# Performance work log

Hardware: AMD Instinct MI355X
Metric: run time of the kernel (lower is better)

## Reference

```python
import jax, jax.numpy as jnp
import numpy as np

B, C, H, W = 32, 3, 512, 512
OUT = (64, 64)  # (out_grid[0]=Nx, out_grid[1]=Ny)
SMALL = 1e-4


def setup_inputs() -> dict:
    key = jax.random.key(0)
    k1, k2 = jax.random.split(key, 2)
    X = jax.random.normal(k1, (B, C, H, W), dtype=jnp.float32)
    fan_in = C * H * W
    # localization net: flatten + dense(5); scaled so p ~ N(0,1) and exp(p) is stable
    W_loc = jax.random.normal(k2, (fan_in, 5), dtype=jnp.float32) / np.float32(np.sqrt(fan_in))
    b_loc = jnp.zeros((5,), dtype=jnp.float32)
    return {"X": X, "W_loc": W_loc, "b_loc": b_loc}


def reference(X, W_loc, b_loc):
    Bn = X.shape[0]
    # locnet: p = flatten(X) @ W_loc + b_loc  -> [B, 5]
    p = X.reshape(Bn, -1) @ W_loc + b_loc

    N = min(OUT)
    gx = OUT[0] * (p[:, 0] + 1.0) / 2.0          # [B]
    gy = OUT[1] * (p[:, 1] + 1.0) / 2.0          # [B]
    sigma2 = jnp.exp(p[:, 2])                    # [B]
    delta = jnp.exp(p[:, 3]) * (max(W, H) - 1) / (N - 1.0)  # [B]
    gamma = jnp.exp(p[:, 4])                     # [B]

    i1 = jnp.arange(OUT[0], dtype=jnp.float32)   # [Nx]
    i2 = jnp.arange(OUT[1], dtype=jnp.float32)   # [Ny]
    a = jnp.arange(W, dtype=jnp.float32)         # [W]
    b = jnp.arange(H, dtype=jnp.float32)         # [H]

    mx = gx[:, None] + delta[:, None] * (i1 - N / 2.0 - 0.5)  # [B, Nx]
    my = gy[:, None] + delta[:, None] * (i2 - N / 2.0 - 0.5)  # [B, Ny]

    Fx = jnp.exp(-((a - mx[:, :, None]) ** 2) / (2.0 * sigma2[:, None, None]))  # [B,Nx,W]
    Fx = Fx / (Fx.sum(axis=-1, keepdims=True) + SMALL)
    Fy = jnp.exp(-((b - my[:, :, None]) ** 2) / (2.0 * sigma2[:, None, None]))  # [B,Ny,H]
    Fy = Fy / (Fy.sum(axis=-1, keepdims=True) + SMALL)

    # glimpse read: gamma * Fy @ X @ Fx^T, done as batched contractions
    Fyx = jnp.einsum('bnh,bchw->bcnw', Fy, X)        # [B,C,Ny,W]
    out = jnp.einsum('bcnw,bmw->bcnm', Fyx, Fx)      # [B,C,Ny,Nx]
    return gamma[:, None, None, None] * out
```

## Files before the change

kernel.cpp:

```cpp
#include <hip/hip_runtime.h>
#include <math.h>

#define B_ 32
#define C_ 3
#define H_ 512
#define W_ 512
#define NOUT 64
#define FAN (C_*H_*W_)

#define CHUNKS 96
#define CELEMS (FAN / CHUNKS)
#define BGROUPS 4

#define P_OFF 0
#define FX_OFF 256
#define FY_OFF (FX_OFF + B_*NOUT*W_)

__global__ __launch_bounds__(256) void k_locnet(const float* __restrict__ X,
                                                const float* __restrict__ Wl,
                                                float* __restrict__ ws) {
    const int chunk = blockIdx.x;
    const int b0 = blockIdx.y * 8;
    const int t = threadIdx.x;

    float acc[8][5] = {};
    const size_t base = (size_t)chunk * CELEMS;

    for (int k = t; k < CELEMS / 4; k += 256) {
        const size_t i0 = base + (size_t)k * 4;
        const float4* W4 = (const float4*)(Wl + i0 * 5);
        float4 w0 = W4[0], w1 = W4[1], w2 = W4[2], w3 = W4[3], w4 = W4[4];
        float wv[20] = {w0.x, w0.y, w0.z, w0.w,
                        w1.x, w1.y, w1.z, w1.w,
                        w2.x, w2.y, w2.z, w2.w,
                        w3.x, w3.y, w3.z, w3.w,
                        w4.x, w4.y, w4.z, w4.w};
        #pragma unroll
        for (int bb = 0; bb < 8; bb++) {
            float4 x = *(const float4*)(X + (size_t)(b0 + bb) * FAN + i0);
            float xv[4] = {x.x, x.y, x.z, x.w};
            #pragma unroll
            for (int e = 0; e < 4; e++)
                #pragma unroll
                for (int j = 0; j < 5; j++)
                    acc[bb][j] += xv[e] * wv[e * 5 + j];
        }
    }

    #pragma unroll
    for (int off = 32; off > 0; off >>= 1)
        #pragma unroll
        for (int bb = 0; bb < 8; bb++)
            #pragma unroll
            for (int j = 0; j < 5; j++)
                acc[bb][j] += __shfl_down(acc[bb][j], off);

    __shared__ float sred[4][40];
    const int wave = t >> 6, lane = t & 63;
    if (lane == 0) {
        #pragma unroll
        for (int bb = 0; bb < 8; bb++)
            #pragma unroll
            for (int j = 0; j < 5; j++)
                sred[wave][bb * 5 + j] = acc[bb][j];
    }
    __syncthreads();
    if (t < 40) {
        float s = sred[0][t] + sred[1][t] + sred[2][t] + sred[3][t];
        atomicAdd(&ws[P_OFF + b0 * 5 + t], s);
    }
}

__global__ __launch_bounds__(256) void k_filters(const float* __restrict__ bl,
                                                 float* __restrict__ ws) {
    const int n = blockIdx.x;
    const int b = blockIdx.y;
    const int which = blockIdx.z;
    const int t = threadIdx.x;

    const float p0 = ws[P_OFF + b * 5 + 0] + bl[0];
    const float p1 = ws[P_OFF + b * 5 + 1] + bl[1];
    const float p2 = ws[P_OFF + b * 5 + 2] + bl[2];
    const float p3 = ws[P_OFF + b * 5 + 3] + bl[3];

    const float g = (which == 0) ? 32.f * (p0 + 1.f) : 32.f * (p1 + 1.f);
    const float sigma2 = expf(p2);
    const float inv2s = 0.5f / sigma2;
    const float delta = expf(p3) * (511.0f / 63.0f);
    const float mean = g + delta * ((float)n - 32.5f);

    float d0 = (float)t - mean;
    float f0 = expf(-d0 * d0 * inv2s);
    float d1 = (float)(t + 256) - mean;
    float f1 = expf(-d1 * d1 * inv2s);

    float s = f0 + f1;
    #pragma unroll
    for (int off = 32; off > 0; off >>= 1) s += __shfl_down(s, off);
    __shared__ float sred[4];
    __shared__ float stot;
    const int wave = t >> 6, lane = t & 63;
    if (lane == 0) sred[wave] = s;
    __syncthreads();
    if (t == 0) stot = sred[0] + sred[1] + sred[2] + sred[3] + 1e-4f;
    __syncthreads();
    const float scale = 1.0f / stot;

    float* dst = ws + (which == 0 ? FX_OFF : FY_OFF) + ((size_t)b * NOUT + n) * W_;
    dst[t] = f0 * scale;
    dst[t + 256] = f1 * scale;
}

__global__ __launch_bounds__(256) void k_glimpse(const float* __restrict__ X,
                                                 const float* __restrict__ bl,
                                                 const float* __restrict__ ws,
                                                 float* __restrict__ out) {
    const int hc = blockIdx.x;
    const int bc = blockIdx.y;
    const int b = bc / 3;
    const int t = threadIdx.x;
    const int th = t >> 4;
    const int tm = t & 15;
    const int hbase = hc * 64;

    __shared__ float lds[2 * 64 * 66];
    float (*Xs)[66]  = (float (*)[66])(lds);
    float (*Fxs)[66] = (float (*)[66])(lds + 64 * 66);
    float (*GsT)[66] = (float (*)[66])(lds);
    float (*Fys)[66] = (float (*)[66])(lds + 64 * 66);

    const float* Xp  = X + (size_t)bc * (H_ * W_) + (size_t)hbase * W_;
    const float* Fxp = ws + FX_OFF + (size_t)b * NOUT * W_;
    const float* Fyp = ws + FY_OFF + (size_t)b * NOUT * W_;

    float g[4][4] = {};

    for (int wt = 0; wt < 8; wt++) {
        const int wbase = wt * 64;
        #pragma unroll
        for (int k = 0; k < 4; k++) {
            int idx = t + 256 * k;
            int row = idx >> 4;
            int wq = idx & 15;
            float4 xf = *(const float4*)(Xp + (size_t)row * W_ + wbase + wq * 4);
            float4 ff = *(const float4*)(Fxp + (size_t)row * W_ + wbase + wq * 4);
            float* xd = &Xs[row][wq * 4];
            xd[0] = xf.x; xd[1] = xf.y; xd[2] = xf.z; xd[3] = xf.w;
            float* fd = &Fxs[row][wq * 4];
            fd[0] = ff.x; fd[1] = ff.y; fd[2] = ff.z; fd[3] = ff.w;
        }
        __syncthreads();
        #pragma unroll 4
        for (int w = 0; w < 64; w += 2) {
            float2 xv[4], fv[4];
            #pragma unroll
            for (int i = 0; i < 4; i++) xv[i] = *(const float2*)&Xs[th + 16 * i][w];
            #pragma unroll
            for (int j = 0; j < 4; j++) fv[j] = *(const float2*)&Fxs[tm + 16 * j][w];
            #pragma unroll
            for (int i = 0; i < 4; i++)
                #pragma unroll
                for (int j = 0; j < 4; j++) {
                    g[i][j] += xv[i].x * fv[j].x;
                    g[i][j] += xv[i].y * fv[j].y;
                }
        }
        __syncthreads();
    }

    #pragma unroll
    for (int i = 0; i < 4; i++)
        #pragma unroll
        for (int j = 0; j < 4; j++)
            GsT[tm + 16 * j][th + 16 * i] = g[i][j];

    #pragma unroll
    for (int k = 0; k < 4; k++) {
        int idx = t + 256 * k;
        int n = idx >> 4;
        int hq = idx & 15;
        float4 ff = *(const float4*)(Fyp + (size_t)n * W_ + hbase + hq * 4);
        float* fd = &Fys[n][hq * 4];
        fd[0] = ff.x; fd[1] = ff.y; fd[2] = ff.z; fd[3] = ff.w;
    }
    __syncthreads();

    float a2[4][4] = {};
    #pragma unroll 4
    for (int hl = 0; hl < 64; hl += 2) {
        float2 fy[4], gv[4];
        #pragma unroll
        for (int i = 0; i < 4; i++) fy[i] = *(const float2*)&Fys[th + 16 * i][hl];
        #pragma unroll
        for (int j = 0; j < 4; j++) gv[j] = *(const float2*)&GsT[tm + 16 * j][hl];
        #pragma unroll
        for (int i = 0; i < 4; i++)
            #pragma unroll
            for (int j = 0; j < 4; j++) {
                a2[i][j] += fy[i].x * gv[j].x;
                a2[i][j] += fy[i].y * gv[j].y;
            }
    }

    const float gamma = expf(ws[P_OFF + b * 5 + 4] + bl[4]);
    float* outp = out + (size_t)bc * (NOUT * NOUT);
    #pragma unroll
    for (int i = 0; i < 4; i++)
        #pragma unroll
        for (int j = 0; j < 4; j++)
            atomicAdd(&outp[(th + 16 * i) * NOUT + (tm + 16 * j)], gamma * a2[i][j]);
}

extern "C" void kernel_launch(void* const* d_in, const int* in_sizes, int n_in,
                              void* d_out, int out_size, void* d_ws, size_t ws_size,
                              hipStream_t stream) {
    const float* X  = (const float*)d_in[0];
    const float* Wl = (const float*)d_in[1];
    const float* bl = (const float*)d_in[2];
    float* out = (float*)d_out;
    float* ws  = (float*)d_ws;

    hipMemsetAsync(ws, 0, 1024, stream);
    hipMemsetAsync(out, 0, (size_t)out_size * sizeof(float), stream);

    k_locnet<<<dim3(CHUNKS, BGROUPS), 256, 0, stream>>>(X, Wl, ws);
    k_filters<<<dim3(NOUT, B_, 2), 256, 0, stream>>>(bl, ws);
    k_glimpse<<<dim3(8, B_ * C_), 256, 0, stream>>>(X, bl, ws, out);
}
```

Before: 245.9 us.

## Use split-bf16 MFMA for glimpse contractions and raise locnet chunk count

Replaces the scalar FP32 outer-product loops in the glimpse kernel with bf16 MFMA 16x16x32 instructions. Each FP32 operand is split into high and low bf16 parts and three MFMAs are issued per product to keep close to FP32 accuracy. Operands are converted and stored as bf16 in LDS with a padded pitch. The locnet kernel's chunk count rises from 96 to 384 for more parallelism, at the cost of more atomic adds. Risks are the extra conversion work and the small precision loss from dropping the low-times-low term.

```diff
diff --git a/kernel.cpp b/kernel.cpp
--- a/kernel.cpp
+++ b/kernel.cpp
@@ -8,13 +8,25 @@
 #define NOUT 64
 #define FAN (C_*H_*W_)
 
-#define CHUNKS 96
+#define CHUNKS 384
 #define CELEMS (FAN / CHUNKS)
 #define BGROUPS 4
 
 #define P_OFF 0
 #define FX_OFF 256
 #define FY_OFF (FX_OFF + B_*NOUT*W_)
+
+typedef __bf16 bf16x8 __attribute__((ext_vector_type(8)));
+typedef float f32x4 __attribute__((ext_vector_type(4)));
+
+__device__ __forceinline__ unsigned short f2bf(float f) {
+    unsigned int u = __float_as_uint(f);
+    u = (u + 0x7FFFu + ((u >> 16) & 1u)) >> 16;
+    return (unsigned short)u;
+}
+__device__ __forceinline__ float bf2f(unsigned short h) {
+    return __uint_as_float(((unsigned int)h) << 16);
+}
 
 __global__ __launch_bounds__(256) void k_locnet(const float* __restrict__ X,
                                                 const float* __restrict__ Wl,
@@ -111,6 +123,10 @@
     dst[t + 256] = f1 * scale;
 }
 
+#define KC 64
+#define PITCH 72
+#define TSZ (64 * PITCH)
+
 __global__ __launch_bounds__(256) void k_glimpse(const float* __restrict__ X,
                                                  const float* __restrict__ bl,
                                                  const float* __restrict__ ws,
@@ -119,96 +135,145 @@
     const int bc = blockIdx.y;
     const int b = bc / 3;
     const int t = threadIdx.x;
-    const int th = t >> 4;
-    const int tm = t & 15;
+    const int lane = t & 63;
+    const int wv = t >> 6;
+    const int l15 = lane & 15;
+    const int quad = lane >> 4;
     const int hbase = hc * 64;
 
-    __shared__ float lds[2 * 64 * 66];
-    float (*Xs)[66]  = (float (*)[66])(lds);
-    float (*Fxs)[66] = (float (*)[66])(lds + 64 * 66);
-    float (*GsT)[66] = (float (*)[66])(lds);
-    float (*Fys)[66] = (float (*)[66])(lds + 64 * 66);
+    __shared__ __align__(16) unsigned short lds[4 * TSZ];
+    unsigned short* Xh = lds;
+    unsigned short* Xl = lds + TSZ;
+    unsigned short* Fh = lds + 2 * TSZ;
+    unsigned short* Fl = lds + 3 * TSZ;
 
     const float* Xp  = X + (size_t)bc * (H_ * W_) + (size_t)hbase * W_;
     const float* Fxp = ws + FX_OFF + (size_t)b * NOUT * W_;
     const float* Fyp = ws + FY_OFF + (size_t)b * NOUT * W_;
 
-    float g[4][4] = {};
+    f32x4 acc[4] = {};
 
     for (int wt = 0; wt < 8; wt++) {
-        const int wbase = wt * 64;
-        #pragma unroll
-        for (int k = 0; k < 4; k++) {
-            int idx = t + 256 * k;
+        const int wbase = wt * KC;
+        #pragma unroll
+        for (int k4 = 0; k4 < 4; k4++) {
+            int idx = t + 256 * k4;
             int row = idx >> 4;
-            int wq = idx & 15;
-            float4 xf = *(const float4*)(Xp + (size_t)row * W_ + wbase + wq * 4);
-            float4 ff = *(const float4*)(Fxp + (size_t)row * W_ + wbase + wq * 4);
-            float* xd = &Xs[row][wq * 4];
-            xd[0] = xf.x; xd[1] = xf.y; xd[2] = xf.z; xd[3] = xf.w;
-            float* fd = &Fxs[row][wq * 4];
-            fd[0] = ff.x; fd[1] = ff.y; fd[2] = ff.z; fd[3] = ff.w;
+            int c4 = (idx & 15) * 4;
+            float4 xv = *(const float4*)(Xp + (size_t)row * W_ + wbase + c4);
+            float4 fv = *(const float4*)(Fxp + (size_t)row * W_ + wbase + c4);
+            float xa[4] = {xv.x, xv.y, xv.z, xv.w};
+            float fa[4] = {fv.x, fv.y, fv.z, fv.w};
+            unsigned int xhp[2], xlp[2], fhp[2], flp[2];
+            #pragma unroll
+            for (int hwd = 0; hwd < 2; hwd++) {
+                unsigned short h0 = f2bf(xa[2*hwd]);
+                unsigned short h1 = f2bf(xa[2*hwd+1]);
+                xhp[hwd] = (unsigned int)h0 | ((unsigned int)h1 << 16);
+                unsigned short l0 = f2bf(xa[2*hwd] - bf2f(h0));
+                unsigned short l1 = f2bf(xa[2*hwd+1] - bf2f(h1));
+                xlp[hwd] = (unsigned int)l0 | ((unsigned int)l1 << 16);
+                unsigned short g0 = f2bf(fa[2*hwd]);
+                unsigned short g1 = f2bf(fa[2*hwd+1]);
+                fhp[hwd] = (unsigned int)g0 | ((unsigned int)g1 << 16);
+                unsigned short m0 = f2bf(fa[2*hwd] - bf2f(g0));
+                unsigned short m1 = f2bf(fa[2*hwd+1] - bf2f(g1));
+                flp[hwd] = (unsigned int)m0 | ((unsigned int)m1 << 16);
+            }
+            int o = row * PITCH + c4;
+            *(uint2*)&Xh[o] = make_uint2(xhp[0], xhp[1]);
+            *(uint2*)&Xl[o] = make_uint2(xlp[0], xlp[1]);
+            *(uint2*)&Fh[o] = make_uint2(fhp[0], fhp[1]);
+            *(uint2*)&Fl[o] = make_uint2(flp[0], flp[1]);
         }
         __syncthreads();
-        #pragma unroll 4
-        for (int w = 0; w < 64; w += 2) {
-            float2 xv[4], fv[4];
-            #pragma unroll
-            for (int i = 0; i < 4; i++) xv[i] = *(const float2*)&Xs[th + 16 * i][w];
-            #pragma unroll
-            for (int j = 0; j < 4; j++) fv[j] = *(const float2*)&Fxs[tm + 16 * j][w];
-            #pragma unroll
-            for (int i = 0; i < 4; i++)
-                #pragma unroll
-                for (int j = 0; j < 4; j++) {
-                    g[i][j] += xv[i].x * fv[j].x;
-                    g[i][j] += xv[i].y * fv[j].y;
-                }
+        #pragma unroll
+        for (int ks = 0; ks < 2; ks++) {
+            const int ko = ks * 32 + quad * 8;
+            bf16x8 ah = *(const bf16x8*)&Xh[(16 * wv + l15) * PITCH + ko];
+            bf16x8 al = *(const bf16x8*)&Xl[(16 * wv + l15) * PITCH + ko];
+            #pragma unroll
+            for (int mt = 0; mt < 4; mt++) {
+                bf16x8 bh = *(const bf16x8*)&Fh[(16 * mt + l15) * PITCH + ko];
+                bf16x8 bl2 = *(const bf16x8*)&Fl[(16 * mt + l15) * PITCH + ko];
+                acc[mt] = __builtin_amdgcn_mfma_f32_16x16x32_bf16(ah, bh, acc[mt], 0, 0, 0);
+                acc[mt] = __builtin_amdgcn_mfma_f32_16x16x32_bf16(al, bh, acc[mt], 0, 0, 0);
+                acc[mt] = __builtin_amdgcn_mfma_f32_16x16x32_bf16(ah, bl2, acc[mt], 0, 0, 0);
+            }
         }
         __syncthreads();
     }
 
     #pragma unroll
-    for (int i = 0; i < 4; i++)
-        #pragma unroll
-        for (int j = 0; j < 4; j++)
-            GsT[tm + 16 * j][th + 16 * i] = g[i][j];
-
-    #pragma unroll
-    for (int k = 0; k < 4; k++) {
-        int idx = t + 256 * k;
+    for (int mt = 0; mt < 4; mt++) {
+        unsigned int ghp[2], glp[2];
+        unsigned short gh[4], gl[4];
+        #pragma unroll
+        for (int r = 0; r < 4; r++) {
+            float g = acc[mt][r];
+            gh[r] = f2bf(g);
+            gl[r] = f2bf(g - bf2f(gh[r]));
+        }
+        ghp[0] = (unsigned int)gh[0] | ((unsigned int)gh[1] << 16);
+        ghp[1] = (unsigned int)gh[2] | ((unsigned int)gh[3] << 16);
+        glp[0] = (unsigned int)gl[0] | ((unsigned int)gl[1] << 16);
+        glp[1] = (unsigned int)gl[2] | ((unsigned int)gl[3] << 16);
+        int m = 16 * mt + l15;
+        int h = 16 * wv + quad * 4;
+        int o = m * PITCH + h;
+        *(uint2*)&Xh[o] = make_uint2(ghp[0], ghp[1]);
+        *(uint2*)&Xl[o] = make_uint2(glp[0], glp[1]);
+    }
+
+    #pragma unroll
+    for (int k4 = 0; k4 < 4; k4++) {
+        int idx = t + 256 * k4;
         int n = idx >> 4;
-        int hq = idx & 15;
-        float4 ff = *(const float4*)(Fyp + (size_t)n * W_ + hbase + hq * 4);
-        float* fd = &Fys[n][hq * 4];
-        fd[0] = ff.x; fd[1] = ff.y; fd[2] = ff.z; fd[3] = ff.w;
-    }
-    __syncthreads();
-
-    float a2[4][4] = {};
-    #pragma unroll 4
-    for (int hl = 0; hl < 64; hl += 2) {
-        float2 fy[4], gv[4];
-        #pragma unroll
-        for (int i = 0; i < 4; i++) fy[i] = *(const float2*)&Fys[th + 16 * i][hl];
-        #pragma unroll
-        for (int j = 0; j < 4; j++) gv[j] = *(const float2*)&GsT[tm + 16 * j][hl];
-        #pragma unroll
-        for (int i = 0; i < 4; i++)
-            #pragma unroll
-            for (int j = 0; j < 4; j++) {
-                a2[i][j] += fy[i].x * gv[j].x;
-                a2[i][j] += fy[i].y * gv[j].y;
-            }
+        int c4 = (idx & 15) * 4;
+        float4 fv = *(const float4*)(Fyp + (size_t)n * W_ + hbase + c4);
+        float fa[4] = {fv.x, fv.y, fv.z, fv.w};
+        unsigned int fhp[2], flp[2];
+        #pragma unroll
+        for (int hwd = 0; hwd < 2; hwd++) {
+            unsigned short g0 = f2bf(fa[2*hwd]);
+            unsigned short g1 = f2bf(fa[2*hwd+1]);
+            fhp[hwd] = (unsigned int)g0 | ((unsigned int)g1 << 16);
+            unsigned short m0 = f2bf(fa[2*hwd] - bf2f(g0));
+            unsigned short m1 = f2bf(fa[2*hwd+1] - bf2f(g1));
+            flp[hwd] = (unsigned int)m0 | ((unsigned int)m1 << 16);
+        }
+        int o = n * PITCH + c4;
+        *(uint2*)&Fh[o] = make_uint2(fhp[0], fhp[1]);
+        *(uint2*)&Fl[o] = make_uint2(flp[0], flp[1]);
+    }
+    __syncthreads();
+
+    f32x4 p[4] = {};
+    #pragma unroll
+    for (int ks = 0; ks < 2; ks++) {
+        const int ko = ks * 32 + quad * 8;
+        bf16x8 yh = *(const bf16x8*)&Fh[(16 * wv + l15) * PITCH + ko];
+        bf16x8 yl = *(const bf16x8*)&Fl[(16 * wv + l15) * PITCH + ko];
+        #pragma unroll
+        for (int mt = 0; mt < 4; mt++) {
+            bf16x8 gh = *(const bf16x8*)&Xh[(16 * mt + l15) * PITCH + ko];
+            bf16x8 gl = *(const bf16x8*)&Xl[(16 * mt + l15) * PITCH + ko];
+            p[mt] = __builtin_amdgcn_mfma_f32_16x16x32_bf16(yh, gh, p[mt], 0, 0, 0);
+            p[mt] = __builtin_amdgcn_mfma_f32_16x16x32_bf16(yl, gh, p[mt], 0, 0, 0);
+            p[mt] = __builtin_amdgcn_mfma_f32_16x16x32_bf16(yh, gl, p[mt], 0, 0, 0);
+        }
     }
 
     const float gamma = expf(ws[P_OFF + b * 5 + 4] + bl[4]);
     float* outp = out + (size_t)bc * (NOUT * NOUT);
     #pragma unroll
-    for (int i = 0; i < 4; i++)
-        #pragma unroll
-        for (int j = 0; j < 4; j++)
-            atomicAdd(&outp[(th + 16 * i) * NOUT + (tm + 16 * j)], gamma * a2[i][j]);
+    for (int mt = 0; mt < 4; mt++)
+        #pragma unroll
+        for (int r = 0; r < 4; r++) {
+            int n = 16 * wv + quad * 4 + r;
+            int m = 16 * mt + l15;
+            atomicAdd(&outp[n * NOUT + m], gamma * p[mt][r]);
+        }
 }
 
 extern "C" void kernel_launch(void* const* d_in, const int* in_sizes, int n_in,
```

New measurement: 213.7 us. 13.1% less time.

## Use split-bf16 MFMA for glimpse contractions and retile locnet reduction

Applied to the files above, without the earlier changes.

The glimpse kernel's two FP32 scalar contractions are replaced with bf16 MFMA 16x16x32 instructions using a hi/lo split (three products) to keep near-fp32 accuracy. The filter kernel now writes Fx/Fy as precomputed hi/lo bf16 arrays, and X is converted on the fly. The locnet kernel processes 16 batches per block over 384 chunks to read each weight element fewer times. The aim is to cut the ALU-bound glimpse time and the weight traffic, at the cost of extra conversions, more registers, and a small precision risk.

```diff
diff --git a/kernel.cpp b/kernel.cpp
--- a/kernel.cpp
+++ b/kernel.cpp
@@ -8,22 +8,46 @@
 #define NOUT 64
 #define FAN (C_*H_*W_)
 
-#define CHUNKS 96
+#define CHUNKS 384
 #define CELEMS (FAN / CHUNKS)
-#define BGROUPS 4
-
-#define P_OFF 0
-#define FX_OFF 256
-#define FY_OFF (FX_OFF + B_*NOUT*W_)
-
-__global__ __launch_bounds__(256) void k_locnet(const float* __restrict__ X,
-                                                const float* __restrict__ Wl,
-                                                float* __restrict__ ws) {
+#define NB 16
+#define BGROUPS (B_ / NB)
+
+#define FXH_OFF 1024
+#define ARR_ELEMS (B_*NOUT*W_)
+
+typedef __bf16 bf16x8 __attribute__((ext_vector_type(8)));
+typedef float f32x4 __attribute__((ext_vector_type(4)));
+
+__device__ __forceinline__ unsigned short f2bf(float f) {
+    unsigned int u = __float_as_uint(f);
+    u = (u + 0x7FFFu + ((u >> 16) & 1u)) >> 16;
+    return (unsigned short)u;
+}
+__device__ __forceinline__ float bf2f(unsigned short h) {
+    return __uint_as_float(((unsigned int)h) << 16);
+}
+__device__ __forceinline__ void cvt_hilo(const float* x, bf16x8* hi, bf16x8* lo) {
+    union { unsigned int u[4]; bf16x8 v; } H, L;
+    #pragma unroll
+    for (int i = 0; i < 4; i++) {
+        unsigned short h0 = f2bf(x[2*i]),  h1 = f2bf(x[2*i+1]);
+        H.u[i] = (unsigned int)h0 | ((unsigned int)h1 << 16);
+        unsigned short l0 = f2bf(x[2*i]   - bf2f(h0));
+        unsigned short l1 = f2bf(x[2*i+1] - bf2f(h1));
+        L.u[i] = (unsigned int)l0 | ((unsigned int)l1 << 16);
+    }
+    *hi = H.v; *lo = L.v;
+}
+
+__global__ __launch_bounds__(256, 3) void k_locnet(const float* __restrict__ X,
+                                                   const float* __restrict__ Wl,
+                                                   float* __restrict__ ws) {
     const int chunk = blockIdx.x;
-    const int b0 = blockIdx.y * 8;
+    const int b0 = blockIdx.y * NB;
     const int t = threadIdx.x;
 
-    float acc[8][5] = {};
+    float acc[NB][5] = {};
     const size_t base = (size_t)chunk * CELEMS;
 
     for (int k = t; k < CELEMS / 4; k += 256) {
@@ -36,7 +60,7 @@
                         w3.x, w3.y, w3.z, w3.w,
                         w4.x, w4.y, w4.z, w4.w};
         #pragma unroll
-        for (int bb = 0; bb < 8; bb++) {
+        for (int bb = 0; bb < NB; bb++) {
             float4 x = *(const float4*)(X + (size_t)(b0 + bb) * FAN + i0);
             float xv[4] = {x.x, x.y, x.z, x.w};
             #pragma unroll
@@ -50,42 +74,45 @@
     #pragma unroll
     for (int off = 32; off > 0; off >>= 1)
         #pragma unroll
-        for (int bb = 0; bb < 8; bb++)
+        for (int bb = 0; bb < NB; bb++)
             #pragma unroll
             for (int j = 0; j < 5; j++)
                 acc[bb][j] += __shfl_down(acc[bb][j], off);
 
-    __shared__ float sred[4][40];
+    __shared__ float sred[4][NB * 5];
     const int wave = t >> 6, lane = t & 63;
     if (lane == 0) {
         #pragma unroll
-        for (int bb = 0; bb < 8; bb++)
+        for (int bb = 0; bb < NB; bb++)
             #pragma unroll
             for (int j = 0; j < 5; j++)
                 sred[wave][bb * 5 + j] = acc[bb][j];
     }
     __syncthreads();
-    if (t < 40) {
+    if (t < NB * 5) {
         float s = sred[0][t] + sred[1][t] + sred[2][t] + sred[3][t];
-        atomicAdd(&ws[P_OFF + b0 * 5 + t], s);
+        atomicAdd(&ws[b0 * 5 + t], s);
     }
 }
 
 __global__ __launch_bounds__(256) void k_filters(const float* __restrict__ bl,
-                                                 float* __restrict__ ws) {
+                                                 void* __restrict__ wsv) {
     const int n = blockIdx.x;
     const int b = blockIdx.y;
     const int which = blockIdx.z;
     const int t = threadIdx.x;
 
-    const float p0 = ws[P_OFF + b * 5 + 0] + bl[0];
-    const float p1 = ws[P_OFF + b * 5 + 1] + bl[1];
-    const float p2 = ws[P_OFF + b * 5 + 2] + bl[2];
-    const float p3 = ws[P_OFF + b * 5 + 3] + bl[3];
+    const float* pw = (const float*)wsv;
+    unsigned short* arrh = (unsigned short*)((char*)wsv + FXH_OFF) + (size_t)which * 2 * ARR_ELEMS;
+    unsigned short* arrl = arrh + ARR_ELEMS;
+
+    const float p0 = pw[b * 5 + 0] + bl[0];
+    const float p1 = pw[b * 5 + 1] + bl[1];
+    const float p2 = pw[b * 5 + 2] + bl[2];
+    const float p3 = pw[b * 5 + 3] + bl[3];
 
     const float g = (which == 0) ? 32.f * (p0 + 1.f) : 32.f * (p1 + 1.f);
-    const float sigma2 = expf(p2);
-    const float inv2s = 0.5f / sigma2;
+    const float inv2s = 0.5f / expf(p2);
     const float delta = expf(p3) * (511.0f / 63.0f);
     const float mean = g + delta * ((float)n - 32.5f);
 
@@ -106,109 +133,108 @@
     __syncthreads();
     const float scale = 1.0f / stot;
 
-    float* dst = ws + (which == 0 ? FX_OFF : FY_OFF) + ((size_t)b * NOUT + n) * W_;
-    dst[t] = f0 * scale;
-    dst[t + 256] = f1 * scale;
-}
+    const size_t o = ((size_t)b * NOUT + n) * W_;
+    float v0 = f0 * scale, v1 = f1 * scale;
+    unsigned short h0 = f2bf(v0), h1 = f2bf(v1);
+    arrh[o + t] = h0;
+    arrh[o + t + 256] = h1;
+    arrl[o + t] = f2bf(v0 - bf2f(h0));
+    arrl[o + t + 256] = f2bf(v1 - bf2f(h1));
+}
+
+#define GP 72
 
 __global__ __launch_bounds__(256) void k_glimpse(const float* __restrict__ X,
                                                  const float* __restrict__ bl,
-                                                 const float* __restrict__ ws,
+                                                 const void* __restrict__ wsv,
                                                  float* __restrict__ out) {
     const int hc = blockIdx.x;
     const int bc = blockIdx.y;
     const int b = bc / 3;
     const int t = threadIdx.x;
-    const int th = t >> 4;
-    const int tm = t & 15;
+    const int lane = t & 63;
+    const int wv = t >> 6;
+    const int l15 = lane & 15;
+    const int quad = lane >> 4;
     const int hbase = hc * 64;
 
-    __shared__ float lds[2 * 64 * 66];
-    float (*Xs)[66]  = (float (*)[66])(lds);
-    float (*Fxs)[66] = (float (*)[66])(lds + 64 * 66);
-    float (*GsT)[66] = (float (*)[66])(lds);
-    float (*Fys)[66] = (float (*)[66])(lds + 64 * 66);
-
-    const float* Xp  = X + (size_t)bc * (H_ * W_) + (size_t)hbase * W_;
-    const float* Fxp = ws + FX_OFF + (size_t)b * NOUT * W_;
-    const float* Fyp = ws + FY_OFF + (size_t)b * NOUT * W_;
-
-    float g[4][4] = {};
-
-    for (int wt = 0; wt < 8; wt++) {
-        const int wbase = wt * 64;
-        #pragma unroll
-        for (int k = 0; k < 4; k++) {
-            int idx = t + 256 * k;
-            int row = idx >> 4;
-            int wq = idx & 15;
-            float4 xf = *(const float4*)(Xp + (size_t)row * W_ + wbase + wq * 4);
-            float4 ff = *(const float4*)(Fxp + (size_t)row * W_ + wbase + wq * 4);
-            float* xd = &Xs[row][wq * 4];
-            xd[0] = xf.x; xd[1] = xf.y; xd[2] = xf.z; xd[3] = xf.w;
-            float* fd = &Fxs[row][wq * 4];
-            fd[0] = ff.x; fd[1] = ff.y; fd[2] = ff.z; fd[3] = ff.w;
-        }
-        __syncthreads();
-        #pragma unroll 4
-        for (int w = 0; w < 64; w += 2) {
-            float2 xv[4], fv[4];
-            #pragma unroll
-            for (int i = 0; i < 4; i++) xv[i] = *(const float2*)&Xs[th + 16 * i][w];
-            #pragma unroll
-            for (int j = 0; j < 4; j++) fv[j] = *(const float2*)&Fxs[tm + 16 * j][w];
-            #pragma unroll
-            for (int i = 0; i < 4; i++)
-                #pragma unroll
-                for (int j = 0; j < 4; j++) {
-                    g[i][j] += xv[i].x * fv[j].x;
-                    g[i][j] += xv[i].y * fv[j].y;
-                }
-        }
-        __syncthreads();
-    }
-
-    #pragma unroll
-    for (int i = 0; i < 4; i++)
-        #pragma unroll
-        for (int j = 0; j < 4; j++)
-            GsT[tm + 16 * j][th + 16 * i] = g[i][j];
-
-    #pragma unroll
-    for (int k = 0; k < 4; k++) {
-        int idx = t + 256 * k;
-        int n = idx >> 4;
-        int hq = idx & 15;
-        float4 ff = *(const float4*)(Fyp + (size_t)n * W_ + hbase + hq * 4);
-        float* fd = &Fys[n][hq * 4];
-        fd[0] = ff.x; fd[1] = ff.y; fd[2] = ff.z; fd[3] = ff.w;
-    }
-    __syncthreads();
-
-    float a2[4][4] = {};
+    const float* pw = (const float*)wsv;
+    const unsigned short* fxh = (const unsigned short*)((const char*)wsv + FXH_OFF) + (size_t)b * NOUT * W_;
+    const unsigned short* fxl = fxh + ARR_ELEMS;
+    const unsigned short* fyh = fxh + 2 * ARR_ELEMS;
+    const unsigned short* fyl = fxh + 3 * ARR_ELEMS;
+
+    __shared__ __align__(16) unsigned short Gh[64 * GP];
+    __shared__ __align__(16) unsigned short Gl[64 * GP];
+
+    const float* Xp = X + (size_t)bc * (H_ * W_);
+
+    f32x4 ahh[4] = {}, axl[4] = {};
+    const size_t arow = (size_t)(hbase + 16 * wv + l15) * W_;
     #pragma unroll 4
-    for (int hl = 0; hl < 64; hl += 2) {
-        float2 fy[4], gv[4];
-        #pragma unroll
-        for (int i = 0; i < 4; i++) fy[i] = *(const float2*)&Fys[th + 16 * i][hl];
-        #pragma unroll
-        for (int j = 0; j < 4; j++) gv[j] = *(const float2*)&GsT[tm + 16 * j][hl];
-        #pragma unroll
-        for (int i = 0; i < 4; i++)
-            #pragma unroll
-            for (int j = 0; j < 4; j++) {
-                a2[i][j] += fy[i].x * gv[j].x;
-                a2[i][j] += fy[i].y * gv[j].y;
-            }
-    }
-
-    const float gamma = expf(ws[P_OFF + b * 5 + 4] + bl[4]);
+    for (int ks = 0; ks < 16; ks++) {
+        const int ko = ks * 32 + quad * 8;
+        float xa[8];
+        *(float4*)&xa[0] = *(const float4*)(Xp + arow + ko);
+        *(float4*)&xa[4] = *(const float4*)(Xp + arow + ko + 4);
+        bf16x8 ah, al;
+        cvt_hilo(xa, &ah, &al);
+        #pragma unroll
+        for (int mt = 0; mt < 4; mt++) {
+            const int fo = (16 * mt + l15) * W_ + ko;
+            bf16x8 bh  = *(const bf16x8*)&fxh[fo];
+            bf16x8 bl2 = *(const bf16x8*)&fxl[fo];
+            ahh[mt] = __builtin_amdgcn_mfma_f32_16x16x32_bf16(ah, bh,  ahh[mt], 0, 0, 0);
+            axl[mt] = __builtin_amdgcn_mfma_f32_16x16x32_bf16(al, bh,  axl[mt], 0, 0, 0);
+            axl[mt] = __builtin_amdgcn_mfma_f32_16x16x32_bf16(ah, bl2, axl[mt], 0, 0, 0);
+        }
+    }
+
+    #pragma unroll
+    for (int mt = 0; mt < 4; mt++) {
+        unsigned short gh[4], gl[4];
+        #pragma unroll
+        for (int r = 0; r < 4; r++) {
+            float g = ahh[mt][r] + axl[mt][r];
+            gh[r] = f2bf(g);
+            gl[r] = f2bf(g - bf2f(gh[r]));
+        }
+        int o = (16 * mt + l15) * GP + 16 * wv + quad * 4;
+        *(uint2*)&Gh[o] = make_uint2((unsigned int)gh[0] | ((unsigned int)gh[1] << 16),
+                                     (unsigned int)gh[2] | ((unsigned int)gh[3] << 16));
+        *(uint2*)&Gl[o] = make_uint2((unsigned int)gl[0] | ((unsigned int)gl[1] << 16),
+                                     (unsigned int)gl[2] | ((unsigned int)gl[3] << 16));
+    }
+    __syncthreads();
+
+    f32x4 ph[4] = {}, px[4] = {};
+    const size_t yrow = (size_t)(16 * wv + l15) * W_ + hbase;
+    #pragma unroll
+    for (int ks = 0; ks < 2; ks++) {
+        const int ko = ks * 32 + quad * 8;
+        bf16x8 yh = *(const bf16x8*)&fyh[yrow + ko];
+        bf16x8 yl = *(const bf16x8*)&fyl[yrow + ko];
+        #pragma unroll
+        for (int mt = 0; mt < 4; mt++) {
+            const int go = (16 * mt + l15) * GP + ko;
+            bf16x8 gh = *(const bf16x8*)&Gh[go];
+            bf16x8 gl = *(const bf16x8*)&Gl[go];
+            ph[mt] = __builtin_amdgcn_mfma_f32_16x16x32_bf16(yh, gh, ph[mt], 0, 0, 0);
+            px[mt] = __builtin_amdgcn_mfma_f32_16x16x32_bf16(yl, gh, px[mt], 0, 0, 0);
+            px[mt] = __builtin_amdgcn_mfma_f32_16x16x32_bf16(yh, gl, px[mt], 0, 0, 0);
+        }
+    }
+
+    const float gamma = expf(pw[b * 5 + 4] + bl[4]);
     float* outp = out + (size_t)bc * (NOUT * NOUT);
     #pragma unroll
-    for (int i = 0; i < 4; i++)
-        #pragma unroll
-        for (int j = 0; j < 4; j++)
-            atomicAdd(&outp[(th + 16 * i) * NOUT + (tm + 16 * j)], gamma * a2[i][j]);
+    for (int mt = 0; mt < 4; mt++)
+        #pragma unroll
+        for (int r = 0; r < 4; r++) {
+            int n = 16 * wv + quad * 4 + r;
+            int m = 16 * mt + l15;
+            atomicAdd(&outp[n * NOUT + m], gamma * (ph[mt][r] + px[mt][r]));
+        }
 }
 
 extern "C" void kernel_launch(void* const* d_in, const int* in_sizes, int n_in,
@@ -224,6 +250,6 @@
     hipMemsetAsync(out, 0, (size_t)out_size * sizeof(float), stream);
 
     k_locnet<<<dim3(CHUNKS, BGROUPS), 256, 0, stream>>>(X, Wl, ws);
-    k_filters<<<dim3(NOUT, B_, 2), 256, 0, stream>>>(bl, ws);
-    k_glimpse<<<dim3(8, B_ * C_), 256, 0, stream>>>(X, bl, ws, out);
-}
+    k_filters<<<dim3(NOUT, B_, 2), 256, 0, stream>>>(bl, d_ws);
+    k_glimpse<<<dim3(8, B_ * C_), 256, 0, stream>>>(X, bl, d_ws, out);
+}
```

Result: no change. 248.8 us (+1.2%).
